# Kernel optimization log

Measured on AMD Instinct MI355X. Metric: run time of the kernel, lower is better.

The kernel has to match this reference:

```python
import jax, jax.numpy as jnp
import numpy as np
import math

NUM_CLASSES = 100000
EMBED = 384
BATCH = 512
S = 64.0
M = 0.5
COS_M = math.cos(M)
SIN_M = math.sin(M)
TH = math.cos(math.pi - M)
MM = math.sin(math.pi - M) * M
EPS = 1e-07


def setup_inputs() -> dict:
    key = jax.random.key(0)
    k1, k2, k3 = jax.random.split(key, 3)
    embeddings = jax.random.normal(k1, (BATCH, EMBED), dtype=jnp.float32)
    labels = jax.random.randint(k2, (BATCH,), 0, NUM_CLASSES, dtype=jnp.int64)
    # xavier_uniform-like init for weight [num_classes, embedding_size]
    limit = math.sqrt(6.0 / (NUM_CLASSES + EMBED))
    weight = jax.random.uniform(k3, (NUM_CLASSES, EMBED), dtype=jnp.float32,
                                minval=-limit, maxval=limit)
    return {"embeddings": embeddings, "labels": labels, "weight": weight}


def reference(embeddings, labels, weight):
    # normalize class weights (note: embeddings are NOT normalized, per source)
    W = weight / jnp.linalg.norm(weight, axis=1, keepdims=True)  # [C, E]
    cos_theta = jnp.clip(embeddings @ W.T, -1.0 + EPS, 1.0 - EPS)  # [B, C]
    sin_theta = jnp.sqrt(1.0 - cos_theta ** 2)
    cos_theta_m = cos_theta * COS_M - sin_theta * SIN_M
    cos_theta_m = jnp.where(cos_theta > TH, cos_theta_m, cos_theta - MM)
    one_hot = jax.nn.one_hot(labels, cos_theta.shape[1], dtype=cos_theta.dtype)
    logits = S * (one_hot * cos_theta_m + (1.0 - one_hot) * cos_theta)
    # mean cross-entropy
    logp = jax.nn.log_softmax(logits, axis=-1)  # [B, C]
    nll = -jnp.take_along_axis(logp, labels[:, None], axis=1)[:, 0]
    return jnp.mean(nll)
```

## Files before the change

### kernel.cpp

```cpp
#include <hip/hip_runtime.h>
#include <hip/hip_bf16.h>
#include <math.h>

#define C_CLASSES 100000
#define EMBED     384
#define BATCH     512
#define S_SCALE   64.0f
#define COS_M_    0.8775825618903728f
#define SIN_M_    0.479425538604203f
#define TH_       (-0.8775825618903728f)
#define MM_       0.2397127693021015f
#define EPS_      1e-7f
#define LOG2E_    1.4426950408889634f
#define LN2_      0.6931471805599453f
#define BIGZ_     92.33261191693459f
#define SK1_      92.33248f

#define CT    64
#define NCH   1563

typedef __attribute__((ext_vector_type(8))) short bf16x8;
typedef __attribute__((ext_vector_type(4))) float f32x4;

__device__ inline ushort f2bf(float f) {
    unsigned u = __float_as_uint(f);
    unsigned r = (u + 0x7fffu + ((u >> 16) & 1u)) >> 16;
    return (ushort)r;
}

__global__ __launch_bounds__(256)
void cvt_pack_e(const float* __restrict__ emb, ushort* __restrict__ eP)
{
    int t = blockIdx.x * 256 + threadIdx.x;
    int lane = t & 63;
    int grp  = t >> 6;
    int tile = grp / 12, ks = grp % 12;
    int lr = lane & 15, lg = lane >> 4;
    int row = tile * 16 + lr;
    int col = ks * 32 + lg * 8;
    const float4* src = (const float4*)(emb + (size_t)row * EMBED + col);
    float4 v0 = src[0], v1 = src[1];
    ushort4 o0, o1;
    o0.x = f2bf(v0.x); o0.y = f2bf(v0.y); o0.z = f2bf(v0.z); o0.w = f2bf(v0.w);
    o1.x = f2bf(v1.x); o1.y = f2bf(v1.y); o1.z = f2bf(v1.z); o1.w = f2bf(v1.w);
    ((ushort4*)eP)[t * 2]     = o0;
    ((ushort4*)eP)[t * 2 + 1] = o1;
}

__global__ __launch_bounds__(512, 4)
void arc_fused64(const ushort* __restrict__ eP, const int* __restrict__ labels,
                 const float* __restrict__ weight,
                 float* __restrict__ psum, float* __restrict__ zlabel)
{
    __shared__ ushort Bl[(CT / 16) * 12 * 512];
    __shared__ int    labL[BATCH];

    const int tid = threadIdx.x;

    const int orig = blockIdx.x;
    const int xcd  = orig & 7;
    const int qq   = NCH >> 3, rr = NCH & 7;
    const int blk  = (xcd < rr ? xcd * (qq + 1)
                               : rr * (qq + 1) + (xcd - rr) * qq) + (orig >> 3);
    const int c0   = blk * CT;

    labL[tid] = labels[tid];

    {
        const int p = tid & 15;
        #pragma unroll
        for (int h = 0; h < 2; ++h) {
            const int c = h * 32 + (tid >> 4);
            int row = c0 + c;
            if (row >= C_CLASSES) row = C_CLASSES - 1;
            const float4* src = (const float4*)(weight + (size_t)row * EMBED) + p;

            float4 wv[6];
            float ss = 0.f;
            #pragma unroll
            for (int i = 0; i < 6; ++i) {
                wv[i] = src[16 * i];
                ss += wv[i].x * wv[i].x + wv[i].y * wv[i].y
                    + wv[i].z * wv[i].z + wv[i].w * wv[i].w;
            }
            ss += __shfl_xor(ss, 1, 64);
            ss += __shfl_xor(ss, 2, 64);
            ss += __shfl_xor(ss, 4, 64);
            ss += __shfl_xor(ss, 8, 64);
            const float inv = (ss > 0.f) ? rsqrtf(ss) : 0.f;

            const int t2 = c >> 4, cl = c & 15;
            #pragma unroll
            for (int i = 0; i < 6; ++i) {
                int q   = p + 16 * i;
                int ks  = q >> 3;
                int lgp = (q >> 1) & 3;
                int jo  = (q & 1) * 4;
                ushort4 o;
                o.x = f2bf(wv[i].x * inv); o.y = f2bf(wv[i].y * inv);
                o.z = f2bf(wv[i].z * inv); o.w = f2bf(wv[i].w * inv);
                int ei = (int)(((t2 * 12 + ks) * 64) + cl + 16 * lgp) * 8 + jo;
                ei ^= (lgp & 3) << 4;
                *(ushort4*)&Bl[ei] = o;
            }
            __builtin_amdgcn_sched_barrier(0);
        }
    }
    __syncthreads();

    const int wid = tid >> 6, l = tid & 63;
    const int lr  = l & 15,  lg = l >> 4;
    const int bxo = (lg & 3) << 4;

    const ushort* abase = eP + ((size_t)(wid * 4) * 12 * 64 + l) * 8;

    f32x4 acc[4][4];
    #pragma unroll
    for (int mt = 0; mt < 4; ++mt)
        #pragma unroll
        for (int nt = 0; nt < 4; ++nt)
            acc[mt][nt] = (f32x4){0.f, 0.f, 0.f, 0.f};

    #pragma unroll
    for (int ks = 0; ks < 12; ++ks) {
        bf16x8 a[4], b[4];
        #pragma unroll
        for (int mt = 0; mt < 4; ++mt)
            a[mt] = *(const bf16x8*)(abase + (mt * 12 + ks) * 512);
        #pragma unroll
        for (int nt = 0; nt < 4; ++nt) {
            int ei = (int)((nt * 12 + ks) * 64 + l) * 8;
            b[nt] = *(const bf16x8*)&Bl[ei ^ bxo];
        }
        #pragma unroll
        for (int mt = 0; mt < 4; ++mt)
            #pragma unroll
            for (int nt = 0; nt < 4; ++nt)
                acc[mt][nt] = __builtin_amdgcn_mfma_f32_16x16x32_bf16(
                    a[mt], b[nt], acc[mt][nt], 0, 0, 0);
    }

    const bool tail = (blk == NCH - 1);
    #pragma unroll
    for (int mt = 0; mt < 4; ++mt) {
        #pragma unroll
        for (int rg = 0; rg < 4; ++rg) {
            const int r   = wid * 64 + mt * 16 + lg * 4 + rg;
            const int lab = labL[r];
            float acc4 = 0.f;
            if (!tail) {
                #pragma unroll
                for (int nt = 0; nt < 4; ++nt) {
                    float cv = acc[mt][nt][rg];
                    cv = fminf(fmaxf(cv, -1.f + EPS_), 1.f - EPS_);
                    acc4 += exp2f(fmaf(cv, SK1_, -BIGZ_));
                }
            } else {
                #pragma unroll
                for (int nt = 0; nt < 4; ++nt) {
                    float cv = acc[mt][nt][rg];
                    cv = fminf(fmaxf(cv, -1.f + EPS_), 1.f - EPS_);
                    float z = fmaf(cv, SK1_, -BIGZ_);
                    int gc = c0 + nt * 16 + lr;
                    if (gc >= C_CLASSES) z = -1e30f;
                    acc4 += exp2f(z);
                }
            }
            int off = lab - c0;
            if (((unsigned)off < 64u) && ((off & 15) == lr)) {
                int ntl = off >> 4;
                float cv = (ntl == 0) ? acc[mt][0][rg]
                         : (ntl == 1) ? acc[mt][1][rg]
                         : (ntl == 2) ? acc[mt][2][rg]
                                      : acc[mt][3][rg];
                cv = fminf(fmaxf(cv, -1.f + EPS_), 1.f - EPS_);
                float plain = exp2f(fmaf(cv, SK1_, -BIGZ_));
                float zm;
                if (cv > TH_) {
                    float sv = sqrtf(fmaxf(1.f - cv * cv, 0.f));
                    zm = S_SCALE * (cv * COS_M_ - sv * SIN_M_);
                } else {
                    zm = S_SCALE * (cv - MM_);
                }
                acc4 += exp2f(fmaf(zm, LOG2E_, -BIGZ_)) - plain;
                zlabel[r] = zm;
            }
            acc4 += __shfl_xor(acc4, 1, 64);
            acc4 += __shfl_xor(acc4, 2, 64);
            acc4 += __shfl_xor(acc4, 4, 64);
            acc4 += __shfl_xor(acc4, 8, 64);
            if (lr == 0) psum[(size_t)blk * BATCH + r] = acc4;
        }
    }
}

__global__ __launch_bounds__(256)
void arc_reduce(const float* __restrict__ psum, const float* __restrict__ zlabel,
                float* __restrict__ rowloss)
{
    const int r = blockIdx.x;
    const int tid = threadIdx.x;
    float s = 0.f;
    for (int k = tid; k < NCH; k += 256)
        s += psum[(size_t)k * BATCH + r];
    #pragma unroll
    for (int d = 1; d < 64; d <<= 1) s += __shfl_xor(s, d, 64);
    __shared__ float ssh[4];
    if ((tid & 63) == 0) ssh[tid >> 6] = s;
    __syncthreads();
    if (tid == 0) {
        float t = ssh[0] + ssh[1] + ssh[2] + ssh[3];
        rowloss[r] = LN2_ * (BIGZ_ + log2f(t)) - zlabel[r];
    }
}

__global__ __launch_bounds__(512)
void arc_mean(const float* __restrict__ rowloss, float* __restrict__ out)
{
    const int tid = threadIdx.x;
    float v = rowloss[tid];
    #pragma unroll
    for (int d = 1; d < 64; d <<= 1) v += __shfl_xor(v, d, 64);
    __shared__ float sv[8];
    if ((tid & 63) == 0) sv[tid >> 6] = v;
    __syncthreads();
    if (tid == 0) {
        float t = 0.f;
        #pragma unroll
        for (int w = 0; w < 8; ++w) t += sv[w];
        out[0] = t / (float)BATCH;
    }
}

extern "C" void kernel_launch(void* const* d_in, const int* in_sizes, int n_in,
                              void* d_out, int out_size, void* d_ws, size_t ws_size,
                              hipStream_t stream)
{
    (void)in_sizes; (void)n_in; (void)out_size; (void)ws_size;
    const float* emb    = (const float*)d_in[0];
    const int*   labels = (const int*)d_in[1];
    const float* weight = (const float*)d_in[2];
    float* out = (float*)d_out;

    float*  psum    = (float*)d_ws;
    float*  zlabel  = psum + (size_t)NCH * BATCH;
    float*  rowloss = zlabel + BATCH;
    ushort* eP      = (ushort*)(rowloss + BATCH);

    cvt_pack_e<<<(BATCH * EMBED / 8) / 256, 256, 0, stream>>>(emb, eP);
    arc_fused64<<<NCH, 512, 0, stream>>>(eP, labels, weight, psum, zlabel);
    arc_reduce<<<BATCH, 256, 0, stream>>>(psum, zlabel, rowloss);
    arc_mean<<<1, 512, 0, stream>>>(rowloss, out);
}
```

Before: 97.35 us.

## Split fused ArcFace kernel into 32-class, half-batch blocks

Halves the class tile to 32 and splits the batch into two 256-row halves, so each 256-thread block handles 32 classes by 256 rows. This gives 6250 smaller blocks, uses less LDS per block and raises occupancy, which is meant to improve latency hiding and load balance. In exchange, every weight row is now loaded and normalized twice (once per batch half), and the partial-sum buffer and reduction pass double in size. Because 100000 divides evenly by 32, the tail masking is also removed.

```diff
diff --git a/kernel.cpp b/kernel.cpp
--- a/kernel.cpp
+++ b/kernel.cpp
@@ -16,8 +16,9 @@
 #define BIGZ_     92.33261191693459f
 #define SK1_      92.33248f
 
-#define CT    64
-#define NCH   1563
+#define CT    32
+#define NCHK  3125
+#define NBLK  (NCHK * 2)
 
 typedef __attribute__((ext_vector_type(8))) short bf16x8;
 typedef __attribute__((ext_vector_type(4))) float f32x4;
@@ -47,33 +48,34 @@
     ((ushort4*)eP)[t * 2 + 1] = o1;
 }
 
-__global__ __launch_bounds__(512, 4)
-void arc_fused64(const ushort* __restrict__ eP, const int* __restrict__ labels,
+__global__ __launch_bounds__(256, 5)
+void arc_fused32(const ushort* __restrict__ eP, const int* __restrict__ labels,
                  const float* __restrict__ weight,
                  float* __restrict__ psum, float* __restrict__ zlabel)
 {
     __shared__ ushort Bl[(CT / 16) * 12 * 512];
-    __shared__ int    labL[BATCH];
+    __shared__ int    labL[256];
 
     const int tid = threadIdx.x;
 
     const int orig = blockIdx.x;
     const int xcd  = orig & 7;
-    const int qq   = NCH >> 3, rr = NCH & 7;
-    const int blk  = (xcd < rr ? xcd * (qq + 1)
+    const int qq   = NBLK >> 3, rr = NBLK & 7;
+    const int bid  = (xcd < rr ? xcd * (qq + 1)
                                : rr * (qq + 1) + (xcd - rr) * qq) + (orig >> 3);
-    const int c0   = blk * CT;
-
-    labL[tid] = labels[tid];
+    const int ck   = bid >> 1;
+    const int mh   = bid & 1;
+    const int c0   = ck * CT;
+
+    labL[tid] = labels[mh * 256 + tid];
 
     {
         const int p = tid & 15;
         #pragma unroll
         for (int h = 0; h < 2; ++h) {
-            const int c = h * 32 + (tid >> 4);
-            int row = c0 + c;
-            if (row >= C_CLASSES) row = C_CLASSES - 1;
-            const float4* src = (const float4*)(weight + (size_t)row * EMBED) + p;
+            const int c = h * 16 + (tid >> 4);
+            const float4* src =
+                (const float4*)(weight + (size_t)(c0 + c) * EMBED) + p;
 
             float4 wv[6];
             float ss = 0.f;
@@ -99,7 +101,7 @@
                 ushort4 o;
                 o.x = f2bf(wv[i].x * inv); o.y = f2bf(wv[i].y * inv);
                 o.z = f2bf(wv[i].z * inv); o.w = f2bf(wv[i].w * inv);
-                int ei = (int)(((t2 * 12 + ks) * 64) + cl + 16 * lgp) * 8 + jo;
+                int ei = (((t2 * 12 + ks) * 64) + cl + 16 * lgp) * 8 + jo;
                 ei ^= (lgp & 3) << 4;
                 *(ushort4*)&Bl[ei] = o;
             }
@@ -112,67 +114,52 @@
     const int lr  = l & 15,  lg = l >> 4;
     const int bxo = (lg & 3) << 4;
 
-    const ushort* abase = eP + ((size_t)(wid * 4) * 12 * 64 + l) * 8;
-
-    f32x4 acc[4][4];
-    #pragma unroll
-    for (int mt = 0; mt < 4; ++mt)
-        #pragma unroll
-        for (int nt = 0; nt < 4; ++nt)
-            acc[mt][nt] = (f32x4){0.f, 0.f, 0.f, 0.f};
+    const ushort* abase = eP + ((size_t)((mh * 16 + wid * 4) * 12) * 64 + l) * 8;
+
+    f32x4 acc[4][2];
+    #pragma unroll
+    for (int mt = 0; mt < 4; ++mt) {
+        acc[mt][0] = (f32x4){0.f, 0.f, 0.f, 0.f};
+        acc[mt][1] = (f32x4){0.f, 0.f, 0.f, 0.f};
+    }
 
     #pragma unroll
     for (int ks = 0; ks < 12; ++ks) {
-        bf16x8 a[4], b[4];
+        bf16x8 a[4], b[2];
         #pragma unroll
         for (int mt = 0; mt < 4; ++mt)
             a[mt] = *(const bf16x8*)(abase + (mt * 12 + ks) * 512);
         #pragma unroll
-        for (int nt = 0; nt < 4; ++nt) {
-            int ei = (int)((nt * 12 + ks) * 64 + l) * 8;
+        for (int nt = 0; nt < 2; ++nt) {
+            int ei = ((nt * 12 + ks) * 64 + l) * 8;
             b[nt] = *(const bf16x8*)&Bl[ei ^ bxo];
         }
         #pragma unroll
-        for (int mt = 0; mt < 4; ++mt)
+        for (int mt = 0; mt < 4; ++mt) {
+            acc[mt][0] = __builtin_amdgcn_mfma_f32_16x16x32_bf16(
+                a[mt], b[0], acc[mt][0], 0, 0, 0);
+            acc[mt][1] = __builtin_amdgcn_mfma_f32_16x16x32_bf16(
+                a[mt], b[1], acc[mt][1], 0, 0, 0);
+        }
+    }
+
+    #pragma unroll
+    for (int mt = 0; mt < 4; ++mt) {
+        #pragma unroll
+        for (int rg = 0; rg < 4; ++rg) {
+            const int rl  = wid * 64 + mt * 16 + lg * 4 + rg;
+            const int r   = mh * 256 + rl;
+            const int lab = labL[rl];
+            float acc4 = 0.f;
             #pragma unroll
-            for (int nt = 0; nt < 4; ++nt)
-                acc[mt][nt] = __builtin_amdgcn_mfma_f32_16x16x32_bf16(
-                    a[mt], b[nt], acc[mt][nt], 0, 0, 0);
-    }
-
-    const bool tail = (blk == NCH - 1);
-    #pragma unroll
-    for (int mt = 0; mt < 4; ++mt) {
-        #pragma unroll
-        for (int rg = 0; rg < 4; ++rg) {
-            const int r   = wid * 64 + mt * 16 + lg * 4 + rg;
-            const int lab = labL[r];
-            float acc4 = 0.f;
-            if (!tail) {
-                #pragma unroll
-                for (int nt = 0; nt < 4; ++nt) {
-                    float cv = acc[mt][nt][rg];
-                    cv = fminf(fmaxf(cv, -1.f + EPS_), 1.f - EPS_);
-                    acc4 += exp2f(fmaf(cv, SK1_, -BIGZ_));
-                }
-            } else {
-                #pragma unroll
-                for (int nt = 0; nt < 4; ++nt) {
-                    float cv = acc[mt][nt][rg];
-                    cv = fminf(fmaxf(cv, -1.f + EPS_), 1.f - EPS_);
-                    float z = fmaf(cv, SK1_, -BIGZ_);
-                    int gc = c0 + nt * 16 + lr;
-                    if (gc >= C_CLASSES) z = -1e30f;
-                    acc4 += exp2f(z);
-                }
+            for (int nt = 0; nt < 2; ++nt) {
+                float cv = acc[mt][nt][rg];
+                cv = fminf(fmaxf(cv, -1.f + EPS_), 1.f - EPS_);
+                acc4 += exp2f(fmaf(cv, SK1_, -BIGZ_));
             }
             int off = lab - c0;
-            if (((unsigned)off < 64u) && ((off & 15) == lr)) {
-                int ntl = off >> 4;
-                float cv = (ntl == 0) ? acc[mt][0][rg]
-                         : (ntl == 1) ? acc[mt][1][rg]
-                         : (ntl == 2) ? acc[mt][2][rg]
-                                      : acc[mt][3][rg];
+            if (((unsigned)off < 32u) && ((off & 15) == lr)) {
+                float cv = (off >> 4) ? acc[mt][1][rg] : acc[mt][0][rg];
                 cv = fminf(fmaxf(cv, -1.f + EPS_), 1.f - EPS_);
                 float plain = exp2f(fmaf(cv, SK1_, -BIGZ_));
                 float zm;
@@ -189,7 +176,7 @@
             acc4 += __shfl_xor(acc4, 2, 64);
             acc4 += __shfl_xor(acc4, 4, 64);
             acc4 += __shfl_xor(acc4, 8, 64);
-            if (lr == 0) psum[(size_t)blk * BATCH + r] = acc4;
+            if (lr == 0) psum[(size_t)ck * BATCH + r] = acc4;
         }
     }
 }
@@ -201,7 +188,7 @@
     const int r = blockIdx.x;
     const int tid = threadIdx.x;
     float s = 0.f;
-    for (int k = tid; k < NCH; k += 256)
+    for (int k = tid; k < NCHK; k += 256)
         s += psum[(size_t)k * BATCH + r];
     #pragma unroll
     for (int d = 1; d < 64; d <<= 1) s += __shfl_xor(s, d, 64);
@@ -243,12 +230,12 @@
     float* out = (float*)d_out;
 
     float*  psum    = (float*)d_ws;
-    float*  zlabel  = psum + (size_t)NCH * BATCH;
+    float*  zlabel  = psum + (size_t)NCHK * BATCH;
     float*  rowloss = zlabel + BATCH;
     ushort* eP      = (ushort*)(rowloss + BATCH);
 
     cvt_pack_e<<<(BATCH * EMBED / 8) / 256, 256, 0, stream>>>(emb, eP);
-    arc_fused64<<<NCH, 512, 0, stream>>>(eP, labels, weight, psum, zlabel);
+    arc_fused32<<<NBLK, 256, 0, stream>>>(eP, labels, weight, psum, zlabel);
     arc_reduce<<<BATCH, 256, 0, stream>>>(psum, zlabel, rowloss);
     arc_mean<<<1, 512, 0, stream>>>(rowloss, out);
 }
```

After: 102.6 us. 1.05x slower.

## Widen class tile to 128 with 1024-thread blocks and 2x8 MFMA tiling

Applied to the files above, without the earlier changes.

Each block now handles 128 classes with 16 waves, and each wave covers 32 batch rows by 128 classes instead of 64 by 64. This halves the number of blocks and the partial-sum array the reduce kernel reads, and halves how often each block re-reads the embedding A operand per class. The weight bf16 conversion now uses the library intrinsic. The trade-offs are more LDS per block, 1024-thread blocks with a launch bound of 4 that squeeze registers, and fewer blocks to spread across CUs.

```diff
diff --git a/kernel.cpp b/kernel.cpp
--- a/kernel.cpp
+++ b/kernel.cpp
@@ -16,8 +16,8 @@
 #define BIGZ_     92.33261191693459f
 #define SK1_      92.33248f
 
-#define CT    64
-#define NCH   1563
+#define CT    128
+#define NCH   782
 
 typedef __attribute__((ext_vector_type(8))) short bf16x8;
 typedef __attribute__((ext_vector_type(4))) float f32x4;
@@ -26,6 +26,11 @@
     unsigned u = __float_as_uint(f);
     unsigned r = (u + 0x7fffu + ((u >> 16) & 1u)) >> 16;
     return (ushort)r;
+}
+
+__device__ inline ushort cvt_bf(float f) {
+    __hip_bfloat16 h = __float2bfloat16(f);
+    return *(ushort*)&h;
 }
 
 __global__ __launch_bounds__(256)
@@ -47,10 +52,10 @@
     ((ushort4*)eP)[t * 2 + 1] = o1;
 }
 
-__global__ __launch_bounds__(512, 4)
-void arc_fused64(const ushort* __restrict__ eP, const int* __restrict__ labels,
-                 const float* __restrict__ weight,
-                 float* __restrict__ psum, float* __restrict__ zlabel)
+__global__ __launch_bounds__(1024, 4)
+void arc_fused128(const ushort* __restrict__ eP, const int* __restrict__ labels,
+                  const float* __restrict__ weight,
+                  float* __restrict__ psum, float* __restrict__ zlabel)
 {
     __shared__ ushort Bl[(CT / 16) * 12 * 512];
     __shared__ int    labL[BATCH];
@@ -64,13 +69,13 @@
                                : rr * (qq + 1) + (xcd - rr) * qq) + (orig >> 3);
     const int c0   = blk * CT;
 
-    labL[tid] = labels[tid];
+    if (tid < BATCH) labL[tid] = labels[tid];
 
     {
         const int p = tid & 15;
         #pragma unroll
         for (int h = 0; h < 2; ++h) {
-            const int c = h * 32 + (tid >> 4);
+            const int c = h * 64 + (tid >> 4);
             int row = c0 + c;
             if (row >= C_CLASSES) row = C_CLASSES - 1;
             const float4* src = (const float4*)(weight + (size_t)row * EMBED) + p;
@@ -97,9 +102,9 @@
                 int lgp = (q >> 1) & 3;
                 int jo  = (q & 1) * 4;
                 ushort4 o;
-                o.x = f2bf(wv[i].x * inv); o.y = f2bf(wv[i].y * inv);
-                o.z = f2bf(wv[i].z * inv); o.w = f2bf(wv[i].w * inv);
-                int ei = (int)(((t2 * 12 + ks) * 64) + cl + 16 * lgp) * 8 + jo;
+                o.x = cvt_bf(wv[i].x * inv); o.y = cvt_bf(wv[i].y * inv);
+                o.z = cvt_bf(wv[i].z * inv); o.w = cvt_bf(wv[i].w * inv);
+                int ei = (((t2 * 12 + ks) * 64) + cl + 16 * lgp) * 8 + jo;
                 ei ^= (lgp & 3) << 4;
                 *(ushort4*)&Bl[ei] = o;
             }
@@ -112,52 +117,48 @@
     const int lr  = l & 15,  lg = l >> 4;
     const int bxo = (lg & 3) << 4;
 
-    const ushort* abase = eP + ((size_t)(wid * 4) * 12 * 64 + l) * 8;
-
-    f32x4 acc[4][4];
-    #pragma unroll
-    for (int mt = 0; mt < 4; ++mt)
-        #pragma unroll
-        for (int nt = 0; nt < 4; ++nt)
+    const ushort* abase = eP + ((size_t)(wid * 2) * 12 * 64 + l) * 8;
+
+    f32x4 acc[2][8];
+    #pragma unroll
+    for (int mt = 0; mt < 2; ++mt)
+        #pragma unroll
+        for (int nt = 0; nt < 8; ++nt)
             acc[mt][nt] = (f32x4){0.f, 0.f, 0.f, 0.f};
 
     #pragma unroll
     for (int ks = 0; ks < 12; ++ks) {
-        bf16x8 a[4], b[4];
-        #pragma unroll
-        for (int mt = 0; mt < 4; ++mt)
-            a[mt] = *(const bf16x8*)(abase + (mt * 12 + ks) * 512);
-        #pragma unroll
-        for (int nt = 0; nt < 4; ++nt) {
-            int ei = (int)((nt * 12 + ks) * 64 + l) * 8;
-            b[nt] = *(const bf16x8*)&Bl[ei ^ bxo];
+        bf16x8 a0 = *(const bf16x8*)(abase + (0 * 12 + ks) * 512);
+        bf16x8 a1 = *(const bf16x8*)(abase + (1 * 12 + ks) * 512);
+        #pragma unroll
+        for (int nt = 0; nt < 8; ++nt) {
+            int ei = ((nt * 12 + ks) * 64 + l) * 8;
+            bf16x8 b = *(const bf16x8*)&Bl[ei ^ bxo];
+            acc[0][nt] = __builtin_amdgcn_mfma_f32_16x16x32_bf16(
+                a0, b, acc[0][nt], 0, 0, 0);
+            acc[1][nt] = __builtin_amdgcn_mfma_f32_16x16x32_bf16(
+                a1, b, acc[1][nt], 0, 0, 0);
         }
-        #pragma unroll
-        for (int mt = 0; mt < 4; ++mt)
-            #pragma unroll
-            for (int nt = 0; nt < 4; ++nt)
-                acc[mt][nt] = __builtin_amdgcn_mfma_f32_16x16x32_bf16(
-                    a[mt], b[nt], acc[mt][nt], 0, 0, 0);
     }
 
     const bool tail = (blk == NCH - 1);
     #pragma unroll
-    for (int mt = 0; mt < 4; ++mt) {
+    for (int mt = 0; mt < 2; ++mt) {
         #pragma unroll
         for (int rg = 0; rg < 4; ++rg) {
-            const int r   = wid * 64 + mt * 16 + lg * 4 + rg;
+            const int r   = wid * 32 + mt * 16 + lg * 4 + rg;
             const int lab = labL[r];
             float acc4 = 0.f;
             if (!tail) {
                 #pragma unroll
-                for (int nt = 0; nt < 4; ++nt) {
+                for (int nt = 0; nt < 8; ++nt) {
                     float cv = acc[mt][nt][rg];
                     cv = fminf(fmaxf(cv, -1.f + EPS_), 1.f - EPS_);
                     acc4 += exp2f(fmaf(cv, SK1_, -BIGZ_));
                 }
             } else {
                 #pragma unroll
-                for (int nt = 0; nt < 4; ++nt) {
+                for (int nt = 0; nt < 8; ++nt) {
                     float cv = acc[mt][nt][rg];
                     cv = fminf(fmaxf(cv, -1.f + EPS_), 1.f - EPS_);
                     float z = fmaf(cv, SK1_, -BIGZ_);
@@ -167,12 +168,12 @@
                 }
             }
             int off = lab - c0;
-            if (((unsigned)off < 64u) && ((off & 15) == lr)) {
+            if (((unsigned)off < (unsigned)CT) && ((off & 15) == lr)) {
                 int ntl = off >> 4;
-                float cv = (ntl == 0) ? acc[mt][0][rg]
-                         : (ntl == 1) ? acc[mt][1][rg]
-                         : (ntl == 2) ? acc[mt][2][rg]
-                                      : acc[mt][3][rg];
+                float cv = acc[mt][0][rg];
+                #pragma unroll
+                for (int nt = 1; nt < 8; ++nt)
+                    cv = (ntl == nt) ? acc[mt][nt][rg] : cv;
                 cv = fminf(fmaxf(cv, -1.f + EPS_), 1.f - EPS_);
                 float plain = exp2f(fmaf(cv, SK1_, -BIGZ_));
                 float zm;
@@ -248,7 +249,7 @@
     ushort* eP      = (ushort*)(rowloss + BATCH);
 
     cvt_pack_e<<<(BATCH * EMBED / 8) / 256, 256, 0, stream>>>(emb, eP);
-    arc_fused64<<<NCH, 512, 0, stream>>>(eP, labels, weight, psum, zlabel);
+    arc_fused128<<<NCH, 1024, 0, stream>>>(eP, labels, weight, psum, zlabel);
     arc_reduce<<<BATCH, 256, 0, stream>>>(psum, zlabel, rowloss);
     arc_mean<<<1, 512, 0, stream>>>(rowloss, out);
 }
```

New measurement: 92.18 us. -5.3%, faster.
